# Kernel optimization log

Hardware: AMD Instinct MI355X
Metric: run time of the kernel (lower is better)

## Reference

```python
import jax, jax.numpy as jnp
import numpy as np

B, N = 128, 2048
DX = 10.0 / 2048.0   # X / N
DT = 5.0e-4          # CFL-consistent timestep


def f_real(u):
    # f(u) = 0.5*u*(3 - u^2) + (300/12)*u^2*(3/4 - 2u + 3/2 u^2 - 1/4 u^4)
    u2 = u * u
    return 0.5 * u * (3.0 - u2) + 25.0 * u2 * (0.75 - 2.0 * u + 1.5 * u2 - 0.25 * u2 * u2)


def dfdu_abs(u):
    # f_real is elementwise, so grad of the sum gives the elementwise derivative,
    # matching torch.autograd.grad(f, u, grad_outputs=ones_like(f))
    return jnp.abs(jax.grad(lambda uu: jnp.sum(f_real(uu)))(u))


def setup_inputs() -> dict:
    key = jax.random.key(0)
    init = jax.random.uniform(key, (B, N), dtype=jnp.float32)  # u in [0,1]
    return {"init": init, "stepnum": 500}


def reference(init, stepnum):
    lam = jnp.float32(DT / DX)

    def step(u_old, _):
        f = f_real(u_old)                      # [B, N]
        a = dfdu_abs(u_old)                    # |f'(u)|, [B, N]
        # local Lax-Friedrichs flux: max over the (j, j+1) pair
        alpha = jnp.maximum(a[:, :-1], a[:, 1:])  # [B, N-1]
        f_half = 0.5 * (f[:, :-1] + f[:, 1:]) - 0.5 * alpha * (u_old[:, 1:] - u_old[:, :-1])
        interior = u_old[:, 1:-1] - lam * (f_half[:, 1:] - f_half[:, :-1])  # [B, N-2]
        # boundary: u[:,0]=u[:,1], u[:,N-1]=u[:,N-2]
        u = jnp.concatenate([interior[:, :1], interior, interior[:, -1:]], axis=1)
        return u, u

    _, traj = jax.lax.scan(step, init, None, length=stepnum - 1)  # [stepnum-1, B, N]
    return jnp.concatenate([init[None], traj], axis=0)            # [stepnum, B, N]
```

## Files before the change

kernel.cpp:

```cpp
#include <hip/hip_runtime.h>

#define NPTS 2048
#define TPB  768
#define CAP  1536
#define OWN  1024

typedef float v2f __attribute__((ext_vector_type(2)));

#define EDGE_BARRIER() do {                                   \
    asm volatile("s_waitcnt lgkmcnt(0)" ::: "memory");        \
    __builtin_amdgcn_s_barrier();                             \
    asm volatile("" ::: "memory");                            \
} while (0)

__device__ __forceinline__ void eval_gp(float u, float& g, float& p) {
    const float uu = u * u;
    float gg = fmaf(uu, -3.125f, 18.75f);
    gg = fmaf(u, gg, -25.25f);
    gg = fmaf(u, gg, 9.375f);
    gg = fmaf(u, gg, 0.75f);
    g = u * gg;
    float pp = fmaf(uu, -37.5f, 150.0f);
    pp = fmaf(u, pp, -151.5f);
    pp = fmaf(u, pp, 37.5f);
    p = fmaf(u, pp, 1.5f);
}

__global__ __launch_bounds__(TPB) void lxf_split(
    const float* __restrict__ init, float* __restrict__ out,
    int nbatch, int nsteps)
{
    __shared__ float Ub[2][CAP];
    __shared__ float Gb[2][CAP];
    __shared__ float Pb[2][CAP];

    const int blk = blockIdx.x;
    const int r   = blk >> 1;
    const int h   = blk & 1;
    const int tid = threadIdx.x;
    const int c0  = 2 * tid;
    const int gb  = h ? 512 : 0;
    const size_t rowoff = (size_t)r * NPTS;
    const float lam = 0.1024f;

    const bool st  = h ? (c0 >= 512) : (c0 < OWN);
    const bool bcL = (h == 0) && (tid == 0);
    const bool bcR = (h == 1) && (tid == TPB - 1);
    const int  hl  = (tid == 0)       ? 0       : c0 - 1;
    const int  hr  = (tid == TPB - 1) ? CAP - 1 : c0 + 2;

    v2f uv = *reinterpret_cast<const v2f*>(init + rowoff + gb + c0);
    float u0 = uv.x, u1 = uv.y;
    float g0, p0, g1, p1;
    eval_gp(u0, g0, p0);
    eval_gp(u1, g1, p1);

    if (st) *reinterpret_cast<v2f*>(out + rowoff + gb + c0) = uv;

    {
        *reinterpret_cast<v2f*>(&Ub[0][c0]) = uv;
        v2f gv; gv.x = g0; gv.y = g1;
        *reinterpret_cast<v2f*>(&Gb[0][c0]) = gv;
        v2f pv; pv.x = p0; pv.y = p1;
        *reinterpret_cast<v2f*>(&Pb[0][c0]) = pv;
    }
    EDGE_BARRIER();

    const size_t stride = (size_t)nbatch * NPTS;
    float* dstw = out + rowoff + gb + c0;

#define STEP(CUR, NXT) do {                                            \
    dstw += stride;                                                    \
    const float uL = Ub[CUR][hl], gL = Gb[CUR][hl], pL = Pb[CUR][hl];  \
    const float uR = Ub[CUR][hr], gR = Gb[CUR][hr], pR = Pb[CUR][hr];  \
                         \
    const float aL = fmaxf(fabsf(pL), fabsf(p0));                      \
    const float aM = fmaxf(fabsf(p0), fabsf(p1));                      \
    const float aR = fmaxf(fabsf(p1), fabsf(pR));                      \
    const float fhL = fmaf(-0.5f * aL, u0 - uL, gL + g0);              \
    const float fhM = fmaf(-0.5f * aM, u1 - u0, g0 + g1);              \
    const float fhR = fmaf(-0.5f * aR, uR - u1, g1 + gR);              \
    float n0 = fmaf(-lam, fhM - fhL, u0);                              \
    float n1 = fmaf(-lam, fhR - fhM, u1);                              \
    if (bcL) n0 = n1;                           \
    if (bcR) n1 = n0;                           \
    eval_gp(n0, g0, p0);                                               \
    eval_gp(n1, g1, p1);                                               \
    v2f nv; nv.x = n0; nv.y = n1;                                      \
    *reinterpret_cast<v2f*>(&Ub[NXT][c0]) = nv;                        \
    v2f ngv; ngv.x = g0; ngv.y = g1;                                   \
    *reinterpret_cast<v2f*>(&Gb[NXT][c0]) = ngv;                       \
    v2f npv; npv.x = p0; npv.y = p1;                                   \
    *reinterpret_cast<v2f*>(&Pb[NXT][c0]) = npv;                       \
    if (st) *reinterpret_cast<v2f*>(dstw) = nv;                        \
    u0 = n0; u1 = n1;                                                  \
    EDGE_BARRIER();                                                    \
} while (0)

    const int S  = nsteps - 1;
    const int P2 = S >> 1;
    for (int i = 0; i < P2; ++i) {
        STEP(0, 1);
        STEP(1, 0);
    }
    if (S & 1) STEP(0, 1);
#undef STEP
}

extern "C" void kernel_launch(void* const* d_in, const int* in_sizes, int n_in,
                              void* d_out, int out_size, void* d_ws, size_t ws_size,
                              hipStream_t stream) {
    const float* init = (const float*)d_in[0];
    float* out = (float*)d_out;

    const int nbatch = in_sizes[0] / NPTS;
    const int nsteps = out_size / in_sizes[0];

    hipLaunchKernelGGL(lxf_split, dim3(2 * nbatch), dim3(TPB), 0, stream,
                       init, out, nbatch, nsteps);
}
```

Baseline: 165.1 us.

## Vectorize flux polynomial with packed FMA and skip halo cells outside dependence cone

The two per-thread polynomial evaluations now use packed two-wide float FMAs, which may map to packed math instructions. Each thread also computes its distance from the owned region and skips the update once its halo cell can no longer influence owned output in the remaining steps. Because the halo shrinks over time, the later steps do less work. The cost is a per-step branch and some wave divergence near the cutoff boundary.

```diff
diff --git a/kernel.cpp b/kernel.cpp
--- a/kernel.cpp
+++ b/kernel.cpp
@@ -3,7 +3,6 @@
 #define NPTS 2048
 #define TPB  768
 #define CAP  1536
-#define OWN  1024
 
 typedef float v2f __attribute__((ext_vector_type(2)));
 
@@ -13,17 +12,27 @@
     asm volatile("" ::: "memory");                            \
 } while (0)
 
-__device__ __forceinline__ void eval_gp(float u, float& g, float& p) {
-    const float uu = u * u;
-    float gg = fmaf(uu, -3.125f, 18.75f);
-    gg = fmaf(u, gg, -25.25f);
-    gg = fmaf(u, gg, 9.375f);
-    gg = fmaf(u, gg, 0.75f);
+__device__ __forceinline__ v2f s2(float x) { v2f v; v.x = x; v.y = x; return v; }
+
+__device__ __forceinline__ v2f fma2(v2f a, v2f b, v2f c) {
+#if __has_builtin(__builtin_elementwise_fma)
+    return __builtin_elementwise_fma(a, b, c);
+#else
+    v2f r; r.x = fmaf(a.x, b.x, c.x); r.y = fmaf(a.y, b.y, c.y); return r;
+#endif
+}
+
+__device__ __forceinline__ void eval_gp2(v2f u, v2f& g, v2f& p) {
+    const v2f uu = u * u;
+    v2f gg = fma2(uu, s2(-3.125f), s2(18.75f));
+    gg = fma2(u, gg, s2(-25.25f));
+    gg = fma2(u, gg, s2(9.375f));
+    gg = fma2(u, gg, s2(0.75f));
     g = u * gg;
-    float pp = fmaf(uu, -37.5f, 150.0f);
-    pp = fmaf(u, pp, -151.5f);
-    pp = fmaf(u, pp, 37.5f);
-    p = fmaf(u, pp, 1.5f);
+    v2f pp = fma2(uu, s2(-37.5f), s2(150.0f));
+    pp = fma2(u, pp, s2(-151.5f));
+    pp = fma2(u, pp, s2(37.5f));
+    p = fma2(u, pp, s2(1.5f));
 }
 
 __global__ __launch_bounds__(TPB) void lxf_split(
@@ -43,61 +52,55 @@
     const size_t rowoff = (size_t)r * NPTS;
     const float lam = 0.1024f;
 
-    const bool st  = h ? (c0 >= 512) : (c0 < OWN);
+    const bool st  = h ? (c0 >= 512) : (c0 < 1024);
     const bool bcL = (h == 0) && (tid == 0);
     const bool bcR = (h == 1) && (tid == TPB - 1);
     const int  hl  = (tid == 0)       ? 0       : c0 - 1;
     const int  hr  = (tid == TPB - 1) ? CAP - 1 : c0 + 2;
+    const int dist = h ? (509 - c0) : (c0 - 1025);
 
     v2f uv = *reinterpret_cast<const v2f*>(init + rowoff + gb + c0);
-    float u0 = uv.x, u1 = uv.y;
-    float g0, p0, g1, p1;
-    eval_gp(u0, g0, p0);
-    eval_gp(u1, g1, p1);
+    v2f gv, pv;
+    eval_gp2(uv, gv, pv);
 
     if (st) *reinterpret_cast<v2f*>(out + rowoff + gb + c0) = uv;
 
-    {
-        *reinterpret_cast<v2f*>(&Ub[0][c0]) = uv;
-        v2f gv; gv.x = g0; gv.y = g1;
-        *reinterpret_cast<v2f*>(&Gb[0][c0]) = gv;
-        v2f pv; pv.x = p0; pv.y = p1;
-        *reinterpret_cast<v2f*>(&Pb[0][c0]) = pv;
-    }
+    *reinterpret_cast<v2f*>(&Ub[0][c0]) = uv;
+    *reinterpret_cast<v2f*>(&Gb[0][c0]) = gv;
+    *reinterpret_cast<v2f*>(&Pb[0][c0]) = pv;
     EDGE_BARRIER();
 
     const size_t stride = (size_t)nbatch * NPTS;
     float* dstw = out + rowoff + gb + c0;
 
-#define STEP(CUR, NXT) do {                                            \
-    dstw += stride;                                                    \
-    const float uL = Ub[CUR][hl], gL = Gb[CUR][hl], pL = Pb[CUR][hl];  \
-    const float uR = Ub[CUR][hr], gR = Gb[CUR][hr], pR = Pb[CUR][hr];  \
-                         \
-    const float aL = fmaxf(fabsf(pL), fabsf(p0));                      \
-    const float aM = fmaxf(fabsf(p0), fabsf(p1));                      \
-    const float aR = fmaxf(fabsf(p1), fabsf(pR));                      \
-    const float fhL = fmaf(-0.5f * aL, u0 - uL, gL + g0);              \
-    const float fhM = fmaf(-0.5f * aM, u1 - u0, g0 + g1);              \
-    const float fhR = fmaf(-0.5f * aR, uR - u1, g1 + gR);              \
-    float n0 = fmaf(-lam, fhM - fhL, u0);                              \
-    float n1 = fmaf(-lam, fhR - fhM, u1);                              \
-    if (bcL) n0 = n1;                           \
-    if (bcR) n1 = n0;                           \
-    eval_gp(n0, g0, p0);                                               \
-    eval_gp(n1, g1, p1);                                               \
-    v2f nv; nv.x = n0; nv.y = n1;                                      \
-    *reinterpret_cast<v2f*>(&Ub[NXT][c0]) = nv;                        \
-    v2f ngv; ngv.x = g0; ngv.y = g1;                                   \
-    *reinterpret_cast<v2f*>(&Gb[NXT][c0]) = ngv;                       \
-    v2f npv; npv.x = p0; npv.y = p1;                                   \
-    *reinterpret_cast<v2f*>(&Pb[NXT][c0]) = npv;                       \
-    if (st) *reinterpret_cast<v2f*>(dstw) = nv;                        \
-    u0 = n0; u1 = n1;                                                  \
-    EDGE_BARRIER();                                                    \
+#define STEP(CUR, NXT) do {                                              \
+    dstw += stride;                                                      \
+    if (dist <= rem) {                                                   \
+        const float uL = Ub[CUR][hl], gL = Gb[CUR][hl], pL = Pb[CUR][hl];\
+        const float uR = Ub[CUR][hr], gR = Gb[CUR][hr], pR = Pb[CUR][hr];\
+        const float aL = fmaxf(fabsf(pL), fabsf(pv.x));                  \
+        const float aM = fmaxf(fabsf(pv.x), fabsf(pv.y));                \
+        const float aR = fmaxf(fabsf(pv.y), fabsf(pR));                  \
+        const float fhL = fmaf(-0.5f * aL, uv.x - uL, gL + gv.x);        \
+        const float fhM = fmaf(-0.5f * aM, uv.y - uv.x, gv.x + gv.y);    \
+        const float fhR = fmaf(-0.5f * aR, uR - uv.y, gv.y + gR);        \
+        float n0 = fmaf(-lam, fhM - fhL, uv.x);                          \
+        float n1 = fmaf(-lam, fhR - fhM, uv.y);                          \
+        if (bcL) n0 = n1;                           \
+        if (bcR) n1 = n0;                           \
+        uv.x = n0; uv.y = n1;                                            \
+        eval_gp2(uv, gv, pv);                                            \
+        *reinterpret_cast<v2f*>(&Ub[NXT][c0]) = uv;                      \
+        *reinterpret_cast<v2f*>(&Gb[NXT][c0]) = gv;                      \
+        *reinterpret_cast<v2f*>(&Pb[NXT][c0]) = pv;                      \
+        if (st) *reinterpret_cast<v2f*>(dstw) = uv;                      \
+    }                                                                    \
+    --rem;                                                               \
+    EDGE_BARRIER();                                                      \
 } while (0)
 
     const int S  = nsteps - 1;
+    int rem = S - 1;
     const int P2 = S >> 1;
     for (int i = 0; i < P2; ++i) {
         STEP(0, 1);
```

New measurement: 157.6 us. 4.5% less time.
